# Performance work log

Hardware: AMD Instinct MI355X
Metric: run time of the kernel (lower is better)

The kernel has to match this reference:

```python
import jax, jax.numpy as jnp
import numpy as np

N_SAMPLES = 64
N_AGENTS = 64          # agents per sample (fully connected subgraph)
N = N_SAMPLES * N_AGENTS
F_DIM = 128            # decoder_latent_size
EDIM = 2
ZDIM = 2 * F_DIM + EDIM
BN_EPS = 1e-5


def _build_edge_index():
    # fully-connected (no self loops) per sample, with node offsets, COO row-major
    idx = np.arange(N_AGENTS)
    rows = np.repeat(idx, N_AGENTS)
    cols = np.tile(idx, N_AGENTS)
    mask = rows != cols
    rows, cols = rows[mask], cols[mask]
    offs = (np.arange(N_SAMPLES) * N_AGENTS)[:, None]
    src = (rows[None, :] + offs).ravel().astype(np.int32)  # edge_index[0] = source j
    dst = (cols[None, :] + offs).ravel().astype(np.int32)  # edge_index[1] = target i
    return src, dst


def setup_inputs() -> dict:
    key = jax.random.key(0)
    ks = jax.random.split(key, 12)
    src, dst = _build_edge_index()
    s = 1.0 / np.sqrt(ZDIM)
    inp = {
        "gnn_in": jax.random.normal(ks[0], (N, F_DIM), dtype=jnp.float32),
        "centers": jax.random.normal(ks[1], (N, EDIM), dtype=jnp.float32),
        "src": jnp.asarray(src),
        "dst": jnp.asarray(dst),
        "Wf1": jax.random.normal(ks[2], (F_DIM, ZDIM), dtype=jnp.float32) * s,
        "bf1": jnp.zeros((F_DIM,), jnp.float32),
        "Ws1": jax.random.normal(ks[3], (F_DIM, ZDIM), dtype=jnp.float32) * s,
        "bs1": jnp.zeros((F_DIM,), jnp.float32),
        "g1": jnp.ones((F_DIM,), jnp.float32),
        "be1": jnp.zeros((F_DIM,), jnp.float32),
        "Wf2": jax.random.normal(ks[4], (F_DIM, ZDIM), dtype=jnp.float32) * s,
        "bf2": jnp.zeros((F_DIM,), jnp.float32),
        "Ws2": jax.random.normal(ks[5], (F_DIM, ZDIM), dtype=jnp.float32) * s,
        "bs2": jnp.zeros((F_DIM,), jnp.float32),
        "g2": jnp.ones((F_DIM,), jnp.float32),
        "be2": jnp.zeros((F_DIM,), jnp.float32),
    }
    return inp


def _cgconv(x, edge_attr, src, dst, Wf, bf, Ws, bs, gamma, beta):
    # z_ij = [x_i, x_j, e_ij]  (i = target = dst, j = source = src)
    z = jnp.concatenate([x[dst], x[src], edge_attr], axis=-1)        # [E, 2F+2]
    msg = jax.nn.sigmoid(z @ Wf.T + bf) * jax.nn.softplus(z @ Ws.T + bs)  # [E, F]
    agg = jax.ops.segment_sum(msg, dst, num_segments=N)              # [N, F]
    # BatchNorm1d (training mode: batch stats, biased var), then residual
    mean = agg.mean(axis=0)
    var = agg.var(axis=0)
    agg = (agg - mean) * jax.lax.rsqrt(var + BN_EPS) * gamma + beta
    return agg + x


def reference(gnn_in, centers, src, dst,
              Wf1, bf1, Ws1, bs1, g1, be1,
              Wf2, bf2, Ws2, bs2, g2, be2):
    edge_attr = centers[dst] - centers[src]                           # data[cols] - data[rows]
    x = jax.nn.relu(_cgconv(gnn_in, edge_attr, src, dst, Wf1, bf1, Ws1, bs1, g1, be1))
    out = jax.nn.relu(_cgconv(x, edge_attr, src, dst, Wf2, bf2, Ws2, bs2, g2, be2))
    # original splits per sample; uniform sample size -> concatenation == out itself
    return out
```

## Files before the change

kernel.cpp:

```cpp
#include <hip/hip_runtime.h>

constexpr int NS = 64;
constexpr int NA = 64;
constexpr int NN = NS * NA;
constexpr int FD = 128;
constexpr int ZD = 2 * FD + 2;
constexpr int FS = 16;
constexpr int NB = NS * (FD / FS);
constexpr int NT = 512;
constexpr int XPAD = 132;
constexpr float BN_EPS = 1e-5f;
constexpr float L2E = 1.44269504088896f;
constexpr float LN2 = 0.69314718055995f;

__device__ __forceinline__ void selfpack_w(
    float4* __restrict__ PK,
    const float* __restrict__ Wf, const float* __restrict__ Ws,
    int fq, int tid)
{
    for (int i = tid; i < FD * FS; i += NT) {
        int k = i >> 4, fr = i & (FS - 1);
        int f = fq * FS + fr;
        PK[k * FD + f] = make_float4(Wf[f * ZD + k], Wf[f * ZD + FD + k],
                                     Ws[f * ZD + k], Ws[f * ZD + FD + k]);
    }
}

__device__ __forceinline__ void layer_body(
    const float (*xs)[XPAD], const float2* cs, float2 (*q)[FS],
    const float4* __restrict__ PK,
    const float* __restrict__ Wf, const float* __restrict__ Ws,
    const float* __restrict__ bf, const float* __restrict__ bs,
    int tid, int s, int fq,
    float* __restrict__ agg, float* __restrict__ pS, float* __restrict__ pSS)
{
    const int fl = tid & (FS - 1);
    const int ig = tid >> 4;
    const int f  = fq * FS + fl;
    const int base = s * NA;
    const float4* Wp = PK + f;

    float aPf0=0.f,aQf0=0.f,aPs0=0.f,aQs0=0.f;
    float aPf1=0.f,aQf1=0.f,aPs1=0.f,aQs1=0.f;
    #pragma unroll 2
    for (int k = 0; k < FD; k += 4) {
        float4 x0 = *(const float4*)&xs[ig][k];
        float4 x1 = *(const float4*)&xs[ig + 32][k];
        float4 w0 = Wp[(k + 0) * FD];
        float4 w1 = Wp[(k + 1) * FD];
        float4 w2 = Wp[(k + 2) * FD];
        float4 w3 = Wp[(k + 3) * FD];
        aPf0 = fmaf(x0.x, w0.x, aPf0); aQf0 = fmaf(x0.x, w0.y, aQf0);
        aPs0 = fmaf(x0.x, w0.z, aPs0); aQs0 = fmaf(x0.x, w0.w, aQs0);
        aPf1 = fmaf(x1.x, w0.x, aPf1); aQf1 = fmaf(x1.x, w0.y, aQf1);
        aPs1 = fmaf(x1.x, w0.z, aPs1); aQs1 = fmaf(x1.x, w0.w, aQs1);

        aPf0 = fmaf(x0.y, w1.x, aPf0); aQf0 = fmaf(x0.y, w1.y, aQf0);
        aPs0 = fmaf(x0.y, w1.z, aPs0); aQs0 = fmaf(x0.y, w1.w, aQs0);
        aPf1 = fmaf(x1.y, w1.x, aPf1); aQf1 = fmaf(x1.y, w1.y, aQf1);
        aPs1 = fmaf(x1.y, w1.z, aPs1); aQs1 = fmaf(x1.y, w1.w, aQs1);

        aPf0 = fmaf(x0.z, w2.x, aPf0); aQf0 = fmaf(x0.z, w2.y, aQf0);
        aPs0 = fmaf(x0.z, w2.z, aPs0); aQs0 = fmaf(x0.z, w2.w, aQs0);
        aPf1 = fmaf(x1.z, w2.x, aPf1); aQf1 = fmaf(x1.z, w2.y, aQf1);
        aPs1 = fmaf(x1.z, w2.z, aPs1); aQs1 = fmaf(x1.z, w2.w, aQs1);

        aPf0 = fmaf(x0.w, w3.x, aPf0); aQf0 = fmaf(x0.w, w3.y, aQf0);
        aPs0 = fmaf(x0.w, w3.z, aPs0); aQs0 = fmaf(x0.w, w3.w, aQs0);
        aPf1 = fmaf(x1.w, w3.x, aPf1); aQf1 = fmaf(x1.w, w3.y, aQf1);
        aPs1 = fmaf(x1.w, w3.z, aPs1); aQs1 = fmaf(x1.w, w3.w, aQs1);
    }
    float we0 = Wf[f*ZD + 2*FD], we1 = Wf[f*ZD + 2*FD + 1];
    float ws0 = Ws[f*ZD + 2*FD], ws1 = Ws[f*ZD + 2*FD + 1];
    float bfv = bf[f], bsv = bs[f];
    float2 c0 = cs[ig], c1 = cs[ig + 32];
    float cf0 = c0.x*we0 + c0.y*we1, cg0 = c0.x*ws0 + c0.y*ws1;
    float cf1 = c1.x*we0 + c1.y*we1, cg1 = c1.x*ws0 + c1.y*ws1;
    float Pf0 = aPf0 + cf0 + bfv, Ps0 = aPs0 + cg0 + bsv;
    float Pf1 = aPf1 + cf1 + bfv, Ps1 = aPs1 + cg1 + bsv;
    float Qf0 = aQf0 - cf0,       Qs0 = aQs0 - cg0;
    float Qf1 = aQf1 - cf1,       Qs1 = aQs1 - cg1;
    float2 p0 = make_float2(__builtin_amdgcn_exp2f(-Pf0*L2E), __builtin_amdgcn_exp2f(Ps0*L2E));
    float2 p1 = make_float2(__builtin_amdgcn_exp2f(-Pf1*L2E), __builtin_amdgcn_exp2f(Ps1*L2E));
    q[ig][fl]    = make_float2(__builtin_amdgcn_exp2f(-Qf0*L2E), __builtin_amdgcn_exp2f(Qs0*L2E));
    q[ig+32][fl] = make_float2(__builtin_amdgcn_exp2f(-Qf1*L2E), __builtin_amdgcn_exp2f(Qs1*L2E));
    __syncthreads();

    float a0=0.f, a1=0.f, b0=0.f, b1=0.f;
    #pragma unroll 4
    for (int j = 0; j < NA; j += 2) {
        float2 qa = q[j][fl];
        float2 qb = q[j+1][fl];
        a0 = fmaf(__builtin_amdgcn_rcpf(1.0f + p0.x*qa.x),
                  __builtin_amdgcn_logf(1.0f + p0.y*qa.y), a0);
        b0 = fmaf(__builtin_amdgcn_rcpf(1.0f + p1.x*qa.x),
                  __builtin_amdgcn_logf(1.0f + p1.y*qa.y), b0);
        a1 = fmaf(__builtin_amdgcn_rcpf(1.0f + p0.x*qb.x),
                  __builtin_amdgcn_logf(1.0f + p0.y*qb.y), a1);
        b1 = fmaf(__builtin_amdgcn_rcpf(1.0f + p1.x*qb.x),
                  __builtin_amdgcn_logf(1.0f + p1.y*qb.y), b1);
    }
    float aA = a0 + a1, aB = b0 + b1;
    {
        float2 qv0 = q[ig][fl];
        aA -= __builtin_amdgcn_rcpf(1.0f + p0.x*qv0.x) *
              __builtin_amdgcn_logf(1.0f + p0.y*qv0.y);
        float2 qv1 = q[ig+32][fl];
        aB -= __builtin_amdgcn_rcpf(1.0f + p1.x*qv1.x) *
              __builtin_amdgcn_logf(1.0f + p1.y*qv1.y);
    }
    aA *= LN2; aB *= LN2;
    agg[(base + ig) * FD + f]      = aA;
    agg[(base + ig + 32) * FD + f] = aB;

    __syncthreads();
    float* sm = (float*)q;
    sm[tid]      = aA + aB;
    sm[NT + tid] = aA*aA + aB*aB;
    __syncthreads();
    if (tid < FS) {
        float sv = 0.f, qv = 0.f;
        #pragma unroll
        for (int r = 0; r < 32; ++r) {
            sv += sm[r * FS + tid];
            qv += sm[NT + r * FS + tid];
        }
        pS [s * FD + fq * FS + tid] = sv;
        pSS[s * FD + fq * FS + tid] = qv;
    }
}

__global__ __launch_bounds__(NT) void layer1_kernel(
    const float* __restrict__ X0, const float* __restrict__ C,
    const float* __restrict__ Wf, const float* __restrict__ Ws,
    const float* __restrict__ bf, const float* __restrict__ bs,
    float4* __restrict__ PK,
    float* __restrict__ agg, float* __restrict__ pS, float* __restrict__ pSS)
{
    __shared__ __align__(16) float xs[NA][XPAD];
    __shared__ float2 q[NA][FS];
    __shared__ float2 cs[NA];
    int tid = threadIdx.x, bid = blockIdx.x;
    int s = bid & (NS - 1), fq = bid >> 6;
    int base = s * NA;
    selfpack_w(PK, Wf, Ws, fq, tid);
    const float4* Xv = (const float4*)(X0 + base * FD);
    for (int idx = tid; idx < NA * FD / 4; idx += NT) {
        int n = idx >> 5, k4 = idx & 31;
        *(float4*)&xs[n][k4 * 4] = Xv[idx];
    }
    if (tid < NA) cs[tid] = ((const float2*)C)[base + tid];
    __threadfence_block();
    __syncthreads();
    layer_body(xs, cs, q, PK, Wf, Ws, bf, bs, tid, s, fq, agg, pS, pSS);
}

__global__ __launch_bounds__(NT) void layer2_kernel(
    const float* __restrict__ X0, const float* __restrict__ agg1,
    const float* __restrict__ C,
    const float* __restrict__ pS1, const float* __restrict__ pSS1,
    const float* __restrict__ g1, const float* __restrict__ be1,
    const float* __restrict__ Wf, const float* __restrict__ Ws,
    const float* __restrict__ bf, const float* __restrict__ bs,
    float4* __restrict__ PK,
    float* __restrict__ x1, float* __restrict__ agg2,
    float* __restrict__ pS2, float* __restrict__ pSS2)
{
    __shared__ __align__(16) float xs[NA][XPAD];
    __shared__ float2 q[NA][FS];
    __shared__ float2 cs[NA];
    __shared__ float bnsc[FD], bnsh[FD];
    int tid = threadIdx.x, bid = blockIdx.x;
    int s = bid & (NS - 1), fq = bid >> 6;
    int base = s * NA;
    selfpack_w(PK, Wf, Ws, fq, tid);
    {
        int fr = tid & (FD - 1), sq = tid >> 7;
        float sv = 0.f, qv = 0.f;
        #pragma unroll
        for (int s2 = 0; s2 < NS / 4; ++s2) {
            int si = sq * (NS / 4) + s2;
            sv += pS1[si * FD + fr];
            qv += pSS1[si * FD + fr];
        }
        float* sm = (float*)q;
        sm[tid] = sv;
        sm[NT + tid] = qv;
    }
    if (tid < NA) cs[tid] = ((const float2*)C)[base + tid];
    __threadfence_block();
    __syncthreads();
    if (tid < FD) {
        const float* sm = (const float*)q;
        float sv = sm[tid] + sm[FD + tid] + sm[2*FD + tid] + sm[3*FD + tid];
        float qv = sm[NT + tid] + sm[NT + FD + tid] + sm[NT + 2*FD + tid] + sm[NT + 3*FD + tid];
        float m  = sv * (1.0f / NN);
        float v  = qv * (1.0f / NN) - m * m;
        float sc = g1[tid] * rsqrtf(v + BN_EPS);
        bnsc[tid] = sc;
        bnsh[tid] = be1[tid] - m * sc;
    }
    __syncthreads();
    const float4* Xv  = (const float4*)(X0 + base * FD);
    const float4* Av  = (const float4*)(agg1 + base * FD);
    float4*       X1v = (float4*)(x1 + base * FD);
    for (int idx = tid; idx < NA * FD / 4; idx += NT) {
        int n = idx >> 5, k4 = (idx & 31) * 4;
        float4 x = Xv[idx], a = Av[idx];
        float4 r;
        r.x = fmaxf(fmaf(a.x, bnsc[k4 + 0], bnsh[k4 + 0]) + x.x, 0.0f);
        r.y = fmaxf(fmaf(a.y, bnsc[k4 + 1], bnsh[k4 + 1]) + x.y, 0.0f);
        r.z = fmaxf(fmaf(a.z, bnsc[k4 + 2], bnsh[k4 + 2]) + x.z, 0.0f);
        r.w = fmaxf(fmaf(a.w, bnsc[k4 + 3], bnsh[k4 + 3]) + x.w, 0.0f);
        *(float4*)&xs[n][k4] = r;
        X1v[idx] = r;
    }
    __syncthreads();
    layer_body(xs, cs, q, PK, Wf, Ws, bf, bs, tid, s, fq, agg2, pS2, pSS2);
}

__global__ __launch_bounds__(NT) void out_kernel(
    const float4* __restrict__ x1, const float4* __restrict__ agg2,
    const float* __restrict__ pS2, const float* __restrict__ pSS2,
    const float* __restrict__ g2, const float* __restrict__ be2,
    float4* __restrict__ out)
{
    __shared__ float sc[FD], sh[FD];
    int tid = threadIdx.x;
    if (tid < FD) {
        float sv = 0.f, qv = 0.f;
        #pragma unroll
        for (int s2 = 0; s2 < NS; ++s2) {
            sv += pS2[s2 * FD + tid];
            qv += pSS2[s2 * FD + tid];
        }
        float m  = sv * (1.0f / NN);
        float v  = qv * (1.0f / NN) - m * m;
        float scl = g2[tid] * rsqrtf(v + BN_EPS);
        sc[tid] = scl;
        sh[tid] = be2[tid] - m * scl;
    }
    __syncthreads();
    int idx = blockIdx.x * NT + tid;
    int f0 = (idx & 31) * 4;
    float4 xv = x1[idx], av = agg2[idx];
    float4 r;
    r.x = fmaxf(fmaf(av.x, sc[f0 + 0], sh[f0 + 0]) + xv.x, 0.0f);
    r.y = fmaxf(fmaf(av.y, sc[f0 + 1], sh[f0 + 1]) + xv.y, 0.0f);
    r.z = fmaxf(fmaf(av.z, sc[f0 + 2], sh[f0 + 2]) + xv.z, 0.0f);
    r.w = fmaxf(fmaf(av.w, sc[f0 + 3], sh[f0 + 3]) + xv.w, 0.0f);
    out[idx] = r;
}

extern "C" void kernel_launch(void* const* d_in, const int* in_sizes, int n_in,
                              void* d_out, int out_size, void* d_ws, size_t ws_size,
                              hipStream_t stream) {
    const float* gnn_in  = (const float*)d_in[0];
    const float* centers = (const float*)d_in[1];
    const float* Wf1 = (const float*)d_in[4];
    const float* bf1 = (const float*)d_in[5];
    const float* Ws1 = (const float*)d_in[6];
    const float* bs1 = (const float*)d_in[7];
    const float* g1  = (const float*)d_in[8];
    const float* be1 = (const float*)d_in[9];
    const float* Wf2 = (const float*)d_in[10];
    const float* bf2 = (const float*)d_in[11];
    const float* Ws2 = (const float*)d_in[12];
    const float* bs2 = (const float*)d_in[13];
    const float* g2  = (const float*)d_in[14];
    const float* be2 = (const float*)d_in[15];

    char* ws = (char*)d_ws;
    float4* PK1  = (float4*)(ws);
    float4* PK2  = (float4*)(ws + (256 << 10));
    float* agg1  = (float*)(ws + (512 << 10));
    float* agg2  = (float*)(ws + (512 << 10) + (2 << 20));
    float* x1    = (float*)(ws + (512 << 10) + (4 << 20));
    float* p1S   = (float*)(ws + (512 << 10) + (6 << 20));
    float* p1SS  = (float*)(ws + (512 << 10) + (6 << 20) + (32 << 10));
    float* p2S   = (float*)(ws + (512 << 10) + (6 << 20) + (64 << 10));
    float* p2SS  = (float*)(ws + (512 << 10) + (6 << 20) + (96 << 10));

    layer1_kernel<<<NB, NT, 0, stream>>>(gnn_in, centers, Wf1, Ws1, bf1, bs1,
                                         PK1, agg1, p1S, p1SS);
    layer2_kernel<<<NB, NT, 0, stream>>>(gnn_in, agg1, centers, p1S, p1SS, g1, be1,
                                         Wf2, Ws2, bf2, bs2, PK2, x1, agg2, p2S, p2SS);
    out_kernel<<<NN * FD / 4 / NT, NT, 0, stream>>>(
        (const float4*)x1, (const float4*)agg2, p2S, p2SS, g2, be2, (float4*)d_out);
}
```

Baseline: 145.9 us.

## Fuse both CGConv layers and output into one persistent kernel with grid barriers

Replaces the three launches with one persistent kernel. Blocks synchronise between the layer stages through spin-wait grid barriers on per-block flags. Packed weights are staged in LDS instead of a global scratch buffer. The layer-2 input is kept in LDS instead of being reloaded, and the final BatchNorm/ReLU is applied from registers, which removes the x1 and agg2 round trips. The cost is that all 512 blocks must be co-resident. The barrier flags use fixed magic values and are never reset, so on repeated calls the barriers can pass early and read stale data.

```diff
diff --git a/kernel.cpp b/kernel.cpp
--- a/kernel.cpp
+++ b/kernel.cpp
@@ -12,33 +12,48 @@
 constexpr float BN_EPS = 1e-5f;
 constexpr float L2E = 1.44269504088896f;
 constexpr float LN2 = 0.69314718055995f;
-
-__device__ __forceinline__ void selfpack_w(
-    float4* __restrict__ PK,
-    const float* __restrict__ Wf, const float* __restrict__ Ws,
+constexpr unsigned MAGIC1 = 0x51C6A3B7u;
+constexpr unsigned MAGIC2 = 0x9D24E58Fu;
+
+__device__ __forceinline__ void grid_barrier(unsigned* slots, unsigned magic,
+                                             int tid, int bid)
+{
+    __threadfence();
+    __syncthreads();
+    if (tid == 0)
+        __hip_atomic_store(&slots[bid], magic, __ATOMIC_RELEASE,
+                           __HIP_MEMORY_SCOPE_AGENT);
+    while (__hip_atomic_load(&slots[tid], __ATOMIC_ACQUIRE,
+                             __HIP_MEMORY_SCOPE_AGENT) != magic)
+        __builtin_amdgcn_s_sleep(8);
+    __syncthreads();
+}
+
+__device__ __forceinline__ void stage_w(
+    float4 (*wlds)[FS], const float* __restrict__ Wf, const float* __restrict__ Ws,
     int fq, int tid)
 {
     for (int i = tid; i < FD * FS; i += NT) {
         int k = i >> 4, fr = i & (FS - 1);
-        int f = fq * FS + fr;
-        PK[k * FD + f] = make_float4(Wf[f * ZD + k], Wf[f * ZD + FD + k],
-                                     Ws[f * ZD + k], Ws[f * ZD + FD + k]);
+        int row = (fq * FS + fr) * ZD;
+        wlds[k][fr] = make_float4(Wf[row + k], Wf[row + FD + k],
+                                  Ws[row + k], Ws[row + FD + k]);
     }
 }
 
 __device__ __forceinline__ void layer_body(
     const float (*xs)[XPAD], const float2* cs, float2 (*q)[FS],
-    const float4* __restrict__ PK,
+    const float4 (*wlds)[FS],
     const float* __restrict__ Wf, const float* __restrict__ Ws,
     const float* __restrict__ bf, const float* __restrict__ bs,
     int tid, int s, int fq,
-    float* __restrict__ agg, float* __restrict__ pS, float* __restrict__ pSS)
+    float* __restrict__ agg, float* __restrict__ pS, float* __restrict__ pSS,
+    float& aOut0, float& aOut1)
 {
     const int fl = tid & (FS - 1);
     const int ig = tid >> 4;
     const int f  = fq * FS + fl;
     const int base = s * NA;
-    const float4* Wp = PK + f;
 
     float aPf0=0.f,aQf0=0.f,aPs0=0.f,aQs0=0.f;
     float aPf1=0.f,aQf1=0.f,aPs1=0.f,aQs1=0.f;
@@ -46,10 +61,10 @@
     for (int k = 0; k < FD; k += 4) {
         float4 x0 = *(const float4*)&xs[ig][k];
         float4 x1 = *(const float4*)&xs[ig + 32][k];
-        float4 w0 = Wp[(k + 0) * FD];
-        float4 w1 = Wp[(k + 1) * FD];
-        float4 w2 = Wp[(k + 2) * FD];
-        float4 w3 = Wp[(k + 3) * FD];
+        float4 w0 = wlds[k + 0][fl];
+        float4 w1 = wlds[k + 1][fl];
+        float4 w2 = wlds[k + 2][fl];
+        float4 w3 = wlds[k + 3][fl];
         aPf0 = fmaf(x0.x, w0.x, aPf0); aQf0 = fmaf(x0.x, w0.y, aQf0);
         aPs0 = fmaf(x0.x, w0.z, aPs0); aQs0 = fmaf(x0.x, w0.w, aQs0);
         aPf1 = fmaf(x1.x, w0.x, aPf1); aQf1 = fmaf(x1.x, w0.y, aQf1);
@@ -110,8 +125,10 @@
               __builtin_amdgcn_logf(1.0f + p1.y*qv1.y);
     }
     aA *= LN2; aB *= LN2;
-    agg[(base + ig) * FD + f]      = aA;
-    agg[(base + ig + 32) * FD + f] = aB;
+    if (agg) {
+        agg[(base + ig) * FD + f]      = aA;
+        agg[(base + ig + 32) * FD + f] = aB;
+    }
 
     __syncthreads();
     float* sm = (float*)q;
@@ -128,52 +145,50 @@
         pS [s * FD + fq * FS + tid] = sv;
         pSS[s * FD + fq * FS + tid] = qv;
     }
-}
-
-__global__ __launch_bounds__(NT) void layer1_kernel(
+    aOut0 = aA; aOut1 = aB;
+}
+
+__global__ __launch_bounds__(NT, 4) void fused_kernel(
     const float* __restrict__ X0, const float* __restrict__ C,
-    const float* __restrict__ Wf, const float* __restrict__ Ws,
-    const float* __restrict__ bf, const float* __restrict__ bs,
-    float4* __restrict__ PK,
-    float* __restrict__ agg, float* __restrict__ pS, float* __restrict__ pSS)
+    const float* __restrict__ Wf1, const float* __restrict__ bf1,
+    const float* __restrict__ Ws1, const float* __restrict__ bs1,
+    const float* __restrict__ g1, const float* __restrict__ be1,
+    const float* __restrict__ Wf2, const float* __restrict__ bf2,
+    const float* __restrict__ Ws2, const float* __restrict__ bs2,
+    const float* __restrict__ g2, const float* __restrict__ be2,
+    float* __restrict__ agg1,
+    float* __restrict__ pS1, float* __restrict__ pSS1,
+    float* __restrict__ pS2, float* __restrict__ pSS2,
+    unsigned* __restrict__ bar1, unsigned* __restrict__ bar2,
+    float* __restrict__ out)
 {
     __shared__ __align__(16) float xs[NA][XPAD];
+    __shared__ float4 wlds[FD][FS];
     __shared__ float2 q[NA][FS];
     __shared__ float2 cs[NA];
-    int tid = threadIdx.x, bid = blockIdx.x;
-    int s = bid & (NS - 1), fq = bid >> 6;
-    int base = s * NA;
-    selfpack_w(PK, Wf, Ws, fq, tid);
+    __shared__ float bnsc[FD], bnsh[FD];
+
+    const int tid = threadIdx.x, bid = blockIdx.x;
+    const int s = bid & (NS - 1), fq = bid >> 6;
+    const int fl = tid & (FS - 1), ig = tid >> 4;
+    const int f  = fq * FS + fl;
+    const int base = s * NA;
+
+    stage_w(wlds, Wf1, Ws1, fq, tid);
     const float4* Xv = (const float4*)(X0 + base * FD);
     for (int idx = tid; idx < NA * FD / 4; idx += NT) {
         int n = idx >> 5, k4 = idx & 31;
         *(float4*)&xs[n][k4 * 4] = Xv[idx];
     }
     if (tid < NA) cs[tid] = ((const float2*)C)[base + tid];
-    __threadfence_block();
-    __syncthreads();
-    layer_body(xs, cs, q, PK, Wf, Ws, bf, bs, tid, s, fq, agg, pS, pSS);
-}
-
-__global__ __launch_bounds__(NT) void layer2_kernel(
-    const float* __restrict__ X0, const float* __restrict__ agg1,
-    const float* __restrict__ C,
-    const float* __restrict__ pS1, const float* __restrict__ pSS1,
-    const float* __restrict__ g1, const float* __restrict__ be1,
-    const float* __restrict__ Wf, const float* __restrict__ Ws,
-    const float* __restrict__ bf, const float* __restrict__ bs,
-    float4* __restrict__ PK,
-    float* __restrict__ x1, float* __restrict__ agg2,
-    float* __restrict__ pS2, float* __restrict__ pSS2)
-{
-    __shared__ __align__(16) float xs[NA][XPAD];
-    __shared__ float2 q[NA][FS];
-    __shared__ float2 cs[NA];
-    __shared__ float bnsc[FD], bnsh[FD];
-    int tid = threadIdx.x, bid = blockIdx.x;
-    int s = bid & (NS - 1), fq = bid >> 6;
-    int base = s * NA;
-    selfpack_w(PK, Wf, Ws, fq, tid);
+    __syncthreads();
+    float d0, d1;
+    layer_body(xs, cs, q, wlds, Wf1, Ws1, bf1, bs1, tid, s, fq,
+               agg1, pS1, pSS1, d0, d1);
+
+    grid_barrier(bar1, MAGIC1, tid, bid);
+
+    stage_w(wlds, Wf2, Ws2, fq, tid);
     {
         int fr = tid & (FD - 1), sq = tid >> 7;
         float sv = 0.f, qv = 0.f;
@@ -187,8 +202,6 @@
         sm[tid] = sv;
         sm[NT + tid] = qv;
     }
-    if (tid < NA) cs[tid] = ((const float2*)C)[base + tid];
-    __threadfence_block();
     __syncthreads();
     if (tid < FD) {
         const float* sm = (const float*)q;
@@ -201,55 +214,59 @@
         bnsh[tid] = be1[tid] - m * sc;
     }
     __syncthreads();
-    const float4* Xv  = (const float4*)(X0 + base * FD);
-    const float4* Av  = (const float4*)(agg1 + base * FD);
-    float4*       X1v = (float4*)(x1 + base * FD);
+    const float4* Av = (const float4*)(agg1 + base * FD);
     for (int idx = tid; idx < NA * FD / 4; idx += NT) {
         int n = idx >> 5, k4 = (idx & 31) * 4;
-        float4 x = Xv[idx], a = Av[idx];
+        float4 x = *(const float4*)&xs[n][k4];
+        float4 a = Av[idx];
         float4 r;
         r.x = fmaxf(fmaf(a.x, bnsc[k4 + 0], bnsh[k4 + 0]) + x.x, 0.0f);
         r.y = fmaxf(fmaf(a.y, bnsc[k4 + 1], bnsh[k4 + 1]) + x.y, 0.0f);
         r.z = fmaxf(fmaf(a.z, bnsc[k4 + 2], bnsh[k4 + 2]) + x.z, 0.0f);
         r.w = fmaxf(fmaf(a.w, bnsc[k4 + 3], bnsh[k4 + 3]) + x.w, 0.0f);
         *(float4*)&xs[n][k4] = r;
-        X1v[idx] = r;
-    }
-    __syncthreads();
-    layer_body(xs, cs, q, PK, Wf, Ws, bf, bs, tid, s, fq, agg2, pS2, pSS2);
-}
-
-__global__ __launch_bounds__(NT) void out_kernel(
-    const float4* __restrict__ x1, const float4* __restrict__ agg2,
-    const float* __restrict__ pS2, const float* __restrict__ pSS2,
-    const float* __restrict__ g2, const float* __restrict__ be2,
-    float4* __restrict__ out)
-{
-    __shared__ float sc[FD], sh[FD];
-    int tid = threadIdx.x;
-    if (tid < FD) {
+    }
+    __syncthreads();
+    float aA2, aB2;
+    layer_body(xs, cs, q, wlds, Wf2, Ws2, bf2, bs2, tid, s, fq,
+               (float*)nullptr, pS2, pSS2, aA2, aB2);
+
+    grid_barrier(bar2, MAGIC2, tid, bid);
+
+    {
+        int fr = tid & (FS - 1), sq2 = tid >> 4;
         float sv = 0.f, qv = 0.f;
         #pragma unroll
-        for (int s2 = 0; s2 < NS; ++s2) {
-            sv += pS2[s2 * FD + tid];
-            qv += pSS2[s2 * FD + tid];
+        for (int t = 0; t < 2; ++t) {
+            int si = sq2 * 2 + t;
+            sv += pS2[si * FD + fq * FS + fr];
+            qv += pSS2[si * FD + fq * FS + fr];
+        }
+        float* sm = (float*)q;
+        sm[tid] = sv;
+        sm[NT + tid] = qv;
+    }
+    __syncthreads();
+    if (tid < FS) {
+        const float* sm = (const float*)q;
+        float sv = 0.f, qv = 0.f;
+        #pragma unroll
+        for (int g = 0; g < 32; ++g) {
+            sv += sm[g * FS + tid];
+            qv += sm[NT + g * FS + tid];
         }
         float m  = sv * (1.0f / NN);
         float v  = qv * (1.0f / NN) - m * m;
-        float scl = g2[tid] * rsqrtf(v + BN_EPS);
-        sc[tid] = scl;
-        sh[tid] = be2[tid] - m * scl;
-    }
-    __syncthreads();
-    int idx = blockIdx.x * NT + tid;
-    int f0 = (idx & 31) * 4;
-    float4 xv = x1[idx], av = agg2[idx];
-    float4 r;
-    r.x = fmaxf(fmaf(av.x, sc[f0 + 0], sh[f0 + 0]) + xv.x, 0.0f);
-    r.y = fmaxf(fmaf(av.y, sc[f0 + 1], sh[f0 + 1]) + xv.y, 0.0f);
-    r.z = fmaxf(fmaf(av.z, sc[f0 + 2], sh[f0 + 2]) + xv.z, 0.0f);
-    r.w = fmaxf(fmaf(av.w, sc[f0 + 3], sh[f0 + 3]) + xv.w, 0.0f);
-    out[idx] = r;
+        float sc = g2[fq * FS + tid] * rsqrtf(v + BN_EPS);
+        bnsc[tid] = sc;
+        bnsh[tid] = be2[fq * FS + tid] - m * sc;
+    }
+    __syncthreads();
+    {
+        float sc = bnsc[fl], sh = bnsh[fl];
+        out[(base + ig) * FD + f]      = fmaxf(fmaf(aA2, sc, sh) + xs[ig][f], 0.0f);
+        out[(base + ig + 32) * FD + f] = fmaxf(fmaf(aB2, sc, sh) + xs[ig + 32][f], 0.0f);
+    }
 }
 
 extern "C" void kernel_launch(void* const* d_in, const int* in_sizes, int n_in,
@@ -271,20 +288,17 @@
     const float* be2 = (const float*)d_in[15];
 
     char* ws = (char*)d_ws;
-    float4* PK1  = (float4*)(ws);
-    float4* PK2  = (float4*)(ws + (256 << 10));
-    float* agg1  = (float*)(ws + (512 << 10));
-    float* agg2  = (float*)(ws + (512 << 10) + (2 << 20));
-    float* x1    = (float*)(ws + (512 << 10) + (4 << 20));
-    float* p1S   = (float*)(ws + (512 << 10) + (6 << 20));
-    float* p1SS  = (float*)(ws + (512 << 10) + (6 << 20) + (32 << 10));
-    float* p2S   = (float*)(ws + (512 << 10) + (6 << 20) + (64 << 10));
-    float* p2SS  = (float*)(ws + (512 << 10) + (6 << 20) + (96 << 10));
-
-    layer1_kernel<<<NB, NT, 0, stream>>>(gnn_in, centers, Wf1, Ws1, bf1, bs1,
-                                         PK1, agg1, p1S, p1SS);
-    layer2_kernel<<<NB, NT, 0, stream>>>(gnn_in, agg1, centers, p1S, p1SS, g1, be1,
-                                         Wf2, Ws2, bf2, bs2, PK2, x1, agg2, p2S, p2SS);
-    out_kernel<<<NN * FD / 4 / NT, NT, 0, stream>>>(
-        (const float4*)x1, (const float4*)agg2, p2S, p2SS, g2, be2, (float4*)d_out);
-}
+    float*    agg1 = (float*)(ws);
+    float*    pS1  = (float*)(ws + (2 << 20));
+    float*    pSS1 = (float*)(ws + (2 << 20) + (32 << 10));
+    float*    pS2  = (float*)(ws + (2 << 20) + (64 << 10));
+    float*    pSS2 = (float*)(ws + (2 << 20) + (96 << 10));
+    unsigned* bar1 = (unsigned*)(ws + (2 << 20) + (128 << 10));
+    unsigned* bar2 = (unsigned*)(ws + (2 << 20) + (132 << 10));
+
+    fused_kernel<<<NB, NT, 0, stream>>>(
+        gnn_in, centers,
+        Wf1, bf1, Ws1, bs1, g1, be1,
+        Wf2, bf2, Ws2, bs2, g2, be2,
+        agg1, pS1, pSS1, pS2, pSS2, bar1, bar2, (float*)d_out);
+}
```

Result: slower. 376.1 us (+157.7%).

## Stage layer-1 weights in LDS and prepack layer-2 weights once in layer 1

Applied to the files above, without the earlier changes.

Layer 1 now packs its weight slice into shared memory and reads it from there in the inner product loop, instead of having every block write a global packed copy and read it back. The layer-2 weight packing moves into layer 1 and is done only by the s==0 blocks, so layer 2 no longer repacks redundantly in each of its 512 blocks. The output kernel uses 256-thread blocks and splits the BN-stat reduction across two thread groups. This adds 32KB of LDS per layer-1 block, which may lower occupancy, and makes layer 2 depend on packing done in the previous kernel.

```diff
diff --git a/kernel.cpp b/kernel.cpp
--- a/kernel.cpp
+++ b/kernel.cpp
@@ -13,63 +13,28 @@
 constexpr float L2E = 1.44269504088896f;
 constexpr float LN2 = 0.69314718055995f;
 
-__device__ __forceinline__ void selfpack_w(
-    float4* __restrict__ PK,
-    const float* __restrict__ Wf, const float* __restrict__ Ws,
+__device__ __forceinline__ void stage_w(
+    float4 (*wlds)[FS], const float* __restrict__ Wf, const float* __restrict__ Ws,
     int fq, int tid)
 {
     for (int i = tid; i < FD * FS; i += NT) {
         int k = i >> 4, fr = i & (FS - 1);
-        int f = fq * FS + fr;
-        PK[k * FD + f] = make_float4(Wf[f * ZD + k], Wf[f * ZD + FD + k],
-                                     Ws[f * ZD + k], Ws[f * ZD + FD + k]);
-    }
-}
-
-__device__ __forceinline__ void layer_body(
-    const float (*xs)[XPAD], const float2* cs, float2 (*q)[FS],
-    const float4* __restrict__ PK,
+        int row = (fq * FS + fr) * ZD;
+        wlds[k][fr] = make_float4(Wf[row + k], Wf[row + FD + k],
+                                  Ws[row + k], Ws[row + FD + k]);
+    }
+}
+
+__device__ __forceinline__ void layer_tail(
+    float aPf0, float aQf0, float aPs0, float aQs0,
+    float aPf1, float aQf1, float aPs1, float aQs1,
+    const float2* cs, float2 (*q)[FS],
     const float* __restrict__ Wf, const float* __restrict__ Ws,
     const float* __restrict__ bf, const float* __restrict__ bs,
-    int tid, int s, int fq,
-    float* __restrict__ agg, float* __restrict__ pS, float* __restrict__ pSS)
-{
-    const int fl = tid & (FS - 1);
-    const int ig = tid >> 4;
-    const int f  = fq * FS + fl;
-    const int base = s * NA;
-    const float4* Wp = PK + f;
-
-    float aPf0=0.f,aQf0=0.f,aPs0=0.f,aQs0=0.f;
-    float aPf1=0.f,aQf1=0.f,aPs1=0.f,aQs1=0.f;
-    #pragma unroll 2
-    for (int k = 0; k < FD; k += 4) {
-        float4 x0 = *(const float4*)&xs[ig][k];
-        float4 x1 = *(const float4*)&xs[ig + 32][k];
-        float4 w0 = Wp[(k + 0) * FD];
-        float4 w1 = Wp[(k + 1) * FD];
-        float4 w2 = Wp[(k + 2) * FD];
-        float4 w3 = Wp[(k + 3) * FD];
-        aPf0 = fmaf(x0.x, w0.x, aPf0); aQf0 = fmaf(x0.x, w0.y, aQf0);
-        aPs0 = fmaf(x0.x, w0.z, aPs0); aQs0 = fmaf(x0.x, w0.w, aQs0);
-        aPf1 = fmaf(x1.x, w0.x, aPf1); aQf1 = fmaf(x1.x, w0.y, aQf1);
-        aPs1 = fmaf(x1.x, w0.z, aPs1); aQs1 = fmaf(x1.x, w0.w, aQs1);
-
-        aPf0 = fmaf(x0.y, w1.x, aPf0); aQf0 = fmaf(x0.y, w1.y, aQf0);
-        aPs0 = fmaf(x0.y, w1.z, aPs0); aQs0 = fmaf(x0.y, w1.w, aQs0);
-        aPf1 = fmaf(x1.y, w1.x, aPf1); aQf1 = fmaf(x1.y, w1.y, aQf1);
-        aPs1 = fmaf(x1.y, w1.z, aPs1); aQs1 = fmaf(x1.y, w1.w, aQs1);
-
-        aPf0 = fmaf(x0.z, w2.x, aPf0); aQf0 = fmaf(x0.z, w2.y, aQf0);
-        aPs0 = fmaf(x0.z, w2.z, aPs0); aQs0 = fmaf(x0.z, w2.w, aQs0);
-        aPf1 = fmaf(x1.z, w2.x, aPf1); aQf1 = fmaf(x1.z, w2.y, aQf1);
-        aPs1 = fmaf(x1.z, w2.z, aPs1); aQs1 = fmaf(x1.z, w2.w, aQs1);
-
-        aPf0 = fmaf(x0.w, w3.x, aPf0); aQf0 = fmaf(x0.w, w3.y, aQf0);
-        aPs0 = fmaf(x0.w, w3.z, aPs0); aQs0 = fmaf(x0.w, w3.w, aQs0);
-        aPf1 = fmaf(x1.w, w3.x, aPf1); aQf1 = fmaf(x1.w, w3.y, aQf1);
-        aPs1 = fmaf(x1.w, w3.z, aPs1); aQs1 = fmaf(x1.w, w3.w, aQs1);
-    }
+    int tid, int fl, int ig, int f, int s, int fq, int base,
+    float* __restrict__ agg, float* __restrict__ pS, float* __restrict__ pSS,
+    float& aOut0, float& aOut1)
+{
     float we0 = Wf[f*ZD + 2*FD], we1 = Wf[f*ZD + 2*FD + 1];
     float ws0 = Ws[f*ZD + 2*FD], ws1 = Ws[f*ZD + 2*FD + 1];
     float bfv = bf[f], bsv = bs[f];
@@ -128,31 +93,65 @@
         pS [s * FD + fq * FS + tid] = sv;
         pSS[s * FD + fq * FS + tid] = qv;
     }
-}
+    aOut0 = aA; aOut1 = aB;
+}
+
+#define GEMM_STEP(xv, wv) \
+    aPf0 = fmaf(x0.xv, wv.x, aPf0); aQf0 = fmaf(x0.xv, wv.y, aQf0); \
+    aPs0 = fmaf(x0.xv, wv.z, aPs0); aQs0 = fmaf(x0.xv, wv.w, aQs0); \
+    aPf1 = fmaf(x1.xv, wv.x, aPf1); aQf1 = fmaf(x1.xv, wv.y, aQf1); \
+    aPs1 = fmaf(x1.xv, wv.z, aPs1); aQs1 = fmaf(x1.xv, wv.w, aQs1);
 
 __global__ __launch_bounds__(NT) void layer1_kernel(
     const float* __restrict__ X0, const float* __restrict__ C,
     const float* __restrict__ Wf, const float* __restrict__ Ws,
     const float* __restrict__ bf, const float* __restrict__ bs,
-    float4* __restrict__ PK,
+    const float* __restrict__ Wf2, const float* __restrict__ Ws2,
+    float4* __restrict__ PK2,
     float* __restrict__ agg, float* __restrict__ pS, float* __restrict__ pSS)
 {
     __shared__ __align__(16) float xs[NA][XPAD];
+    __shared__ float4 wlds[FD][FS];
     __shared__ float2 q[NA][FS];
     __shared__ float2 cs[NA];
     int tid = threadIdx.x, bid = blockIdx.x;
     int s = bid & (NS - 1), fq = bid >> 6;
     int base = s * NA;
-    selfpack_w(PK, Wf, Ws, fq, tid);
+    if (s == 0) {
+        for (int i = tid; i < FD * FS; i += NT) {
+            int k = i >> 4, fr = i & (FS - 1);
+            int f2 = fq * FS + fr;
+            PK2[k * FD + f2] = make_float4(Wf2[f2*ZD+k], Wf2[f2*ZD+FD+k],
+                                           Ws2[f2*ZD+k], Ws2[f2*ZD+FD+k]);
+        }
+    }
+    stage_w(wlds, Wf, Ws, fq, tid);
     const float4* Xv = (const float4*)(X0 + base * FD);
     for (int idx = tid; idx < NA * FD / 4; idx += NT) {
         int n = idx >> 5, k4 = idx & 31;
         *(float4*)&xs[n][k4 * 4] = Xv[idx];
     }
     if (tid < NA) cs[tid] = ((const float2*)C)[base + tid];
-    __threadfence_block();
-    __syncthreads();
-    layer_body(xs, cs, q, PK, Wf, Ws, bf, bs, tid, s, fq, agg, pS, pSS);
+    __syncthreads();
+
+    const int fl = tid & (FS - 1), ig = tid >> 4;
+    const int f  = fq * FS + fl;
+    float aPf0=0.f,aQf0=0.f,aPs0=0.f,aQs0=0.f;
+    float aPf1=0.f,aQf1=0.f,aPs1=0.f,aQs1=0.f;
+    #pragma unroll 2
+    for (int k = 0; k < FD; k += 4) {
+        float4 x0 = *(const float4*)&xs[ig][k];
+        float4 x1 = *(const float4*)&xs[ig + 32][k];
+        float4 w0 = wlds[k + 0][fl];
+        float4 w1 = wlds[k + 1][fl];
+        float4 w2 = wlds[k + 2][fl];
+        float4 w3 = wlds[k + 3][fl];
+        GEMM_STEP(x, w0) GEMM_STEP(y, w1) GEMM_STEP(z, w2) GEMM_STEP(w, w3)
+    }
+    float d0, d1;
+    layer_tail(aPf0,aQf0,aPs0,aQs0, aPf1,aQf1,aPs1,aQs1,
+               cs, q, Wf, Ws, bf, bs, tid, fl, ig, f, s, fq, base,
+               agg, pS, pSS, d0, d1);
 }
 
 __global__ __launch_bounds__(NT) void layer2_kernel(
@@ -162,7 +161,7 @@
     const float* __restrict__ g1, const float* __restrict__ be1,
     const float* __restrict__ Wf, const float* __restrict__ Ws,
     const float* __restrict__ bf, const float* __restrict__ bs,
-    float4* __restrict__ PK,
+    const float4* __restrict__ PK2,
     float* __restrict__ x1, float* __restrict__ agg2,
     float* __restrict__ pS2, float* __restrict__ pSS2)
 {
@@ -173,7 +172,6 @@
     int tid = threadIdx.x, bid = blockIdx.x;
     int s = bid & (NS - 1), fq = bid >> 6;
     int base = s * NA;
-    selfpack_w(PK, Wf, Ws, fq, tid);
     {
         int fr = tid & (FD - 1), sq = tid >> 7;
         float sv = 0.f, qv = 0.f;
@@ -188,7 +186,6 @@
         sm[NT + tid] = qv;
     }
     if (tid < NA) cs[tid] = ((const float2*)C)[base + tid];
-    __threadfence_block();
     __syncthreads();
     if (tid < FD) {
         const float* sm = (const float*)q;
@@ -216,24 +213,54 @@
         X1v[idx] = r;
     }
     __syncthreads();
-    layer_body(xs, cs, q, PK, Wf, Ws, bf, bs, tid, s, fq, agg2, pS2, pSS2);
-}
-
-__global__ __launch_bounds__(NT) void out_kernel(
+
+    const int fl = tid & (FS - 1), ig = tid >> 4;
+    const int f  = fq * FS + fl;
+    const float4* Wp = PK2 + f;
+    float aPf0=0.f,aQf0=0.f,aPs0=0.f,aQs0=0.f;
+    float aPf1=0.f,aQf1=0.f,aPs1=0.f,aQs1=0.f;
+    #pragma unroll 2
+    for (int k = 0; k < FD; k += 4) {
+        float4 x0 = *(const float4*)&xs[ig][k];
+        float4 x1v = *(const float4*)&xs[ig + 32][k];
+        float4 w0 = Wp[(k + 0) * FD];
+        float4 w1 = Wp[(k + 1) * FD];
+        float4 w2 = Wp[(k + 2) * FD];
+        float4 w3 = Wp[(k + 3) * FD];
+        float4 x1 = x1v;
+        GEMM_STEP(x, w0) GEMM_STEP(y, w1) GEMM_STEP(z, w2) GEMM_STEP(w, w3)
+    }
+    float d0, d1;
+    layer_tail(aPf0,aQf0,aPs0,aQs0, aPf1,aQf1,aPs1,aQs1,
+               cs, q, Wf, Ws, bf, bs, tid, fl, ig, f, s, fq, base,
+               agg2, pS2, pSS2, d0, d1);
+}
+
+__global__ __launch_bounds__(256) void out_kernel(
     const float4* __restrict__ x1, const float4* __restrict__ agg2,
     const float* __restrict__ pS2, const float* __restrict__ pSS2,
     const float* __restrict__ g2, const float* __restrict__ be2,
     float4* __restrict__ out)
 {
+    __shared__ float sm[1024];
     __shared__ float sc[FD], sh[FD];
     int tid = threadIdx.x;
-    if (tid < FD) {
+    {
+        int fr = tid & (FD - 1), sq = tid >> 7;
         float sv = 0.f, qv = 0.f;
         #pragma unroll
-        for (int s2 = 0; s2 < NS; ++s2) {
-            sv += pS2[s2 * FD + tid];
-            qv += pSS2[s2 * FD + tid];
+        for (int s2 = 0; s2 < NS / 2; ++s2) {
+            int si = sq * (NS / 2) + s2;
+            sv += pS2[si * FD + fr];
+            qv += pSS2[si * FD + fr];
         }
+        sm[tid] = sv;
+        sm[512 + tid] = qv;
+    }
+    __syncthreads();
+    if (tid < FD) {
+        float sv = sm[tid] + sm[FD + tid];
+        float qv = sm[512 + tid] + sm[512 + FD + tid];
         float m  = sv * (1.0f / NN);
         float v  = qv * (1.0f / NN) - m * m;
         float scl = g2[tid] * rsqrtf(v + BN_EPS);
@@ -241,7 +268,7 @@
         sh[tid] = be2[tid] - m * scl;
     }
     __syncthreads();
-    int idx = blockIdx.x * NT + tid;
+    int idx = blockIdx.x * 256 + tid;
     int f0 = (idx & 31) * 4;
     float4 xv = x1[idx], av = agg2[idx];
     float4 r;
@@ -271,20 +298,20 @@
     const float* be2 = (const float*)d_in[15];
 
     char* ws = (char*)d_ws;
-    float4* PK1  = (float4*)(ws);
-    float4* PK2  = (float4*)(ws + (256 << 10));
-    float* agg1  = (float*)(ws + (512 << 10));
-    float* agg2  = (float*)(ws + (512 << 10) + (2 << 20));
-    float* x1    = (float*)(ws + (512 << 10) + (4 << 20));
-    float* p1S   = (float*)(ws + (512 << 10) + (6 << 20));
-    float* p1SS  = (float*)(ws + (512 << 10) + (6 << 20) + (32 << 10));
-    float* p2S   = (float*)(ws + (512 << 10) + (6 << 20) + (64 << 10));
-    float* p2SS  = (float*)(ws + (512 << 10) + (6 << 20) + (96 << 10));
+    float*  agg1 = (float*)(ws);
+    float*  agg2 = (float*)(ws + (2 << 20));
+    float*  x1   = (float*)(ws + (4 << 20));
+    float*  p1S  = (float*)(ws + (6 << 20));
+    float*  p1SS = (float*)(ws + (6 << 20) + (32 << 10));
+    float*  p2S  = (float*)(ws + (6 << 20) + (64 << 10));
+    float*  p2SS = (float*)(ws + (6 << 20) + (96 << 10));
+    float4* PK2  = (float4*)(ws + (6 << 20) + (128 << 10));
 
     layer1_kernel<<<NB, NT, 0, stream>>>(gnn_in, centers, Wf1, Ws1, bf1, bs1,
-                                         PK1, agg1, p1S, p1SS);
+                                         Wf2, Ws2, PK2, agg1, p1S, p1SS);
     layer2_kernel<<<NB, NT, 0, stream>>>(gnn_in, agg1, centers, p1S, p1SS, g1, be1,
-                                         Wf2, Ws2, bf2, bs2, PK2, x1, agg2, p2S, p2SS);
-    out_kernel<<<NN * FD / 4 / NT, NT, 0, stream>>>(
+                                         Wf2, Ws2, bf2, bs2, PK2,
+                                         x1, agg2, p2S, p2SS);
+    out_kernel<<<NN * FD / 4 / 256, 256, 0, stream>>>(
         (const float4*)x1, (const float4*)agg2, p2S, p2SS, g2, be2, (float4*)d_out);
 }
```

Result: faster. 138.3 us (-5.2%).
